# Kernel optimization log

Hardware: AMD Instinct MI355X
Metric: run time of the kernel (lower is better)

## Reference

```python
import jax, jax.numpy as jnp
import numpy as np
from jax import lax

# Quantization bit-widths per the module: QuantAct(16) on input,
# QuantConv2d(precision[0]=8), QuantAct(precision[0]+3=11) after relu1,
# QuantLinear(precision[1]=8).
INPUT_BIT = 16
CONV_W_BIT = 8
RELU_BIT = 11
DENSE_W_BIT = 8
EPS = 1e-8


def round_ste(x):
    # straight-through estimator rounding (HAWQ SymmetricQuantFunction)
    return x + lax.stop_gradient(jnp.round(x) - x)


def quant_act(x, bit):
    """Per-tensor symmetric dynamic activation quantization (HAWQ QuantAct).
    Returns fake-quantized x and its scaling factor."""
    n = 2 ** (bit - 1) - 1
    scale = lax.stop_gradient(jnp.maximum(jnp.max(jnp.abs(x)), EPS) / n)
    x_q = jnp.clip(round_ste(x / scale), -n, n) * scale
    return x_q, scale


def quant_weight(w, bit):
    """Per-output-channel symmetric weight quantization. w: [out, ...].
    Returns integer-valued weights and per-channel scale [out]."""
    n = 2 ** (bit - 1) - 1
    absmax = jnp.max(jnp.abs(w.reshape(w.shape[0], -1)), axis=1)
    sf = lax.stop_gradient(jnp.maximum(absmax, EPS) / n)
    bshape = (w.shape[0],) + (1,) * (w.ndim - 1)
    w_int = jnp.clip(round_ste(w / sf.reshape(bshape)), -n, n)
    return w_int, sf


def quant_conv2d(x, p_sf, w, b, bit, stride, pad):
    w_int, w_sf = quant_weight(w, bit)          # [O,I,kh,kw], [O]
    x_int = x / p_sf                            # integer-valued activations
    out_int = lax.conv_general_dilated(
        x_int, w_int, window_strides=(stride, stride),
        padding=((pad, pad), (pad, pad)),
        dimension_numbers=("NCHW", "OIHW", "NCHW"))
    bias_sf = p_sf * w_sf                       # [O]
    b_int = round_ste(b / bias_sf)
    out = (out_int + b_int[None, :, None, None]) * bias_sf[None, :, None, None]
    return out, w_sf


def quant_linear(x, p_sf, w, b, bit):
    w_int, w_sf = quant_weight(w, bit)          # [O,I], [O]
    x_int = x / p_sf
    bias_sf = p_sf * w_sf                       # [O]
    b_int = round_ste(b / bias_sf)
    out = (jnp.einsum("bi,oi->bo", x_int, w_int) + b_int[None, :]) * bias_sf[None, :]
    return out


def setup_inputs() -> dict:
    key = jax.random.key(0)
    k1, k2, k3, k4, k5 = jax.random.split(key, 5)
    B, Cin, H, W = 256, 3, 64, 64
    Cout, K = 64, 3
    Fin, Fout = Cout * 32 * 32, 256  # stride-2 conv -> 32x32 spatial
    x = jax.random.normal(k1, (B, Cin, H, W), dtype=jnp.float32)
    conv_w = jax.random.normal(k2, (Cout, Cin, K, K), dtype=jnp.float32) * 0.1
    conv_b = jax.random.normal(k3, (Cout,), dtype=jnp.float32) * 0.01
    dense_w = jax.random.normal(k4, (Fout, Fin), dtype=jnp.float32) * 0.02
    dense_b = jax.random.normal(k5, (Fout,), dtype=jnp.float32) * 0.01
    return {"x": x, "conv_w": conv_w, "conv_b": conv_b,
            "dense_w": dense_w, "dense_b": dense_b}


def reference(x, conv_w, conv_b, dense_w, dense_b):
    # x, p_sf = quant_input(x)
    xq, p_sf = quant_act(x, INPUT_BIT)
    # x, w_sf = conv(x, p_sf)
    h, w_sf = quant_conv2d(xq, p_sf, conv_w, conv_b, CONV_W_BIT, stride=2, pad=1)
    # relu1
    h = jax.nn.relu(h)
    # x, p_sf = quant_relu(x, p_sf, w_sf)  (requantize at relu_bit)
    h, p_sf = quant_act(h, RELU_BIT)
    # flatten
    h = h.reshape(h.shape[0], -1)
    # relu2(enc_dense(x, p_sf))
    out = jax.nn.relu(quant_linear(h, p_sf, dense_w, dense_b, DENSE_W_BIT))
    return out
```

## Files before the change

kernel.cpp:

```cpp
#include <hip/hip_runtime.h>
#include <hip/hip_fp16.h>
#include <cstdint>

#define B_   256
#define CIN  3
#define HW_  64
#define COUT 64
#define FIN  65536
#define FOUT 256

#define ACC_F    0
#define SC_F     65536
#define XPART_F  65552
#define WPART_F  66064
#define CSF_F    67088
#define CWINT_F  67152
#define H16_BYTE (512*1024)

typedef _Float16 half8  __attribute__((ext_vector_type(8)));
typedef _Float16 half4v __attribute__((ext_vector_type(4)));
typedef float    floatx4 __attribute__((ext_vector_type(4)));
typedef unsigned short u16;

__device__ inline float blockMax(float v) {
    #pragma unroll
    for (int off = 32; off; off >>= 1) v = fmaxf(v, __shfl_down(v, off));
    __shared__ float sm[8];
    const int lane = threadIdx.x & 63, w = threadIdx.x >> 6;
    if (lane == 0) sm[w] = v;
    __syncthreads();
    float m = sm[0];
    const int nw = blockDim.x >> 6;
    for (int i = 1; i < nw; i++) m = fmaxf(m, sm[i]);
    return m;
}

__global__ __launch_bounds__(256) void k_stats(const float* __restrict__ x,
                                               const float* __restrict__ dw,
                                               const float* __restrict__ cw,
                                               float* __restrict__ ws) {
    const int b = blockIdx.x;
    const int t = threadIdx.x;
    if (b < 512) {
        const float4* x4 = (const float4*)x;
        float m = 0.f;
        for (int i = b * 256 + t; i < (B_ * CIN * HW_ * HW_) / 4; i += 512 * 256) {
            float4 v = x4[i];
            m = fmaxf(m, fmaxf(fmaxf(fabsf(v.x), fabsf(v.y)), fmaxf(fabsf(v.z), fabsf(v.w))));
        }
        float bm = blockMax(m);
        if (t == 0) ws[XPART_F + b] = bm;
    } else if (b < 1536) {
        const int b2 = b - 512;
        const int row = b2 >> 2, q = b2 & 3;
        const float4* r = (const float4*)(dw + (size_t)row * FIN) + q * 4096;
        float m = 0.f;
        for (int i = t; i < 4096; i += 256) {
            float4 v = r[i];
            m = fmaxf(m, fmaxf(fmaxf(fabsf(v.x), fabsf(v.y)), fmaxf(fabsf(v.z), fabsf(v.w))));
        }
        float bm = blockMax(m);
        if (t == 0) ws[WPART_F + b2] = bm;
    } else if (b == 1536) {
        if (t == 64) ((unsigned*)ws)[SC_F + 1] = 0u;
        if (t < 64) {
            const int o = t;
            float wv[27];
            float m = 0.f;
            #pragma unroll
            for (int i = 0; i < 27; i++) { wv[i] = cw[o * 27 + i]; m = fmaxf(m, fabsf(wv[i])); }
            const float sf = fmaxf(m, 1e-8f) / 127.0f;
            #pragma unroll
            for (int i = 0; i < 27; i++)
                ws[CWINT_F + o * 27 + i] = fminf(127.f, fmaxf(-127.f, rintf(wv[i] / sf)));
            ws[CSF_F + o] = sf;
        }
    } else {
        ws[ACC_F + (b - 1537) * 256 + t] = 0.f;
    }
}

__global__ __launch_bounds__(256) void k_conv(const float* __restrict__ x,
                                              const float* __restrict__ cb,
                                              const float* __restrict__ ws,
                                              u16* __restrict__ h16,
                                              unsigned* __restrict__ maxh) {
    __shared__ float s_bsf[64], s_bint[64];
    __shared__ float xt[27 * 68];
    __shared__ float xp[256 * 28];
    const int t = threadIdx.x;

    float pm = fmaxf(ws[XPART_F + t], ws[XPART_F + 256 + t]);
    pm = blockMax(pm);
    const float p_sf = fmaxf(pm, 1e-8f) / 32767.0f;
    const float inv_p = 1.0f / p_sf;
    if (t < 64) {
        const float bsf = p_sf * ws[CSF_F + t];
        s_bsf[t]  = bsf;
        s_bint[t] = rintf(cb[t] / bsf);
    }

    const int b   = blockIdx.x >> 3;
    const int oyt = (blockIdx.x & 7) * 4;
    const float* xb = x + (size_t)b * (CIN * HW_ * HW_);

    for (int i = t; i < 432; i += 256) {
        const int lrow = i >> 4, c4 = i & 15;
        const int ci = lrow / 9, lr = lrow - ci * 9;
        const int iy = 2 * oyt - 1 + lr;
        float4 v = make_float4(0.f, 0.f, 0.f, 0.f);
        if ((unsigned)iy < 64u) v = *(const float4*)(xb + (ci * HW_ + iy) * HW_ + c4 * 4);
        float* d = &xt[lrow * 68 + 1 + c4 * 4];
        d[0] = fminf(32767.f, fmaxf(-32767.f, rintf(v.x * inv_p)));
        d[1] = fminf(32767.f, fmaxf(-32767.f, rintf(v.y * inv_p)));
        d[2] = fminf(32767.f, fmaxf(-32767.f, rintf(v.z * inv_p)));
        d[3] = fminf(32767.f, fmaxf(-32767.f, rintf(v.w * inv_p)));
    }
    if (t < 27) xt[t * 68] = 0.f;
    else if (t < 54) xt[(t - 27) * 68 + 65] = 0.f;
    __syncthreads();

    const int ox = t & 31;
    const int ch = __builtin_amdgcn_readfirstlane((t >> 6) & 1);
    const int dy = ((t >> 7) << 1) + ((t >> 5) & 1);
    const int oy = oyt + dy;

    float* myp = &xp[t * 28];
    #pragma unroll
    for (int ci = 0; ci < 3; ci++)
        #pragma unroll
        for (int ky = 0; ky < 3; ky++) {
            const float* rowp = &xt[(ci * 9 + 2 * dy + ky) * 68 + 2 * ox];
            #pragma unroll
            for (int kx = 0; kx < 3; kx++)
                myp[ci * 9 + ky * 3 + kx] = rowp[kx];
        }
    floatx4 xv0 = *(const floatx4*)(myp + 0);
    floatx4 xv1 = *(const floatx4*)(myp + 4);
    floatx4 xv2 = *(const floatx4*)(myp + 8);
    floatx4 xv3 = *(const floatx4*)(myp + 12);
    floatx4 xv4 = *(const floatx4*)(myp + 16);
    floatx4 xv5 = *(const floatx4*)(myp + 20);
    floatx4 xv6 = *(const floatx4*)(myp + 24);
    asm volatile("" : "+v"(xv0), "+v"(xv1), "+v"(xv2), "+v"(xv3),
                      "+v"(xv4), "+v"(xv5), "+v"(xv6));
    float xs[27];
    #pragma unroll
    for (int k = 0; k < 27; k++) {
        const int q = k >> 2, r = k & 3;
        xs[k] = (q == 0) ? xv0[r] : (q == 1) ? xv1[r] : (q == 2) ? xv2[r] :
                (q == 3) ? xv3[r] : (q == 4) ? xv4[r] : (q == 5) ? xv5[r] : xv6[r];
    }

    const float* wr = ws + CWINT_F + ch * (32 * 27);
    float mx = 0.f;
    u16* outp = h16 + (size_t)b * FIN + (size_t)ch * 32 * 1024 + oy * 32 + ox;

    float wbuf[27];
    #pragma unroll
    for (int k = 0; k < 27; k++) wbuf[k] = wr[k];
    #pragma unroll
    for (int c = 0; c < 32; c++) {
        float wcur[27];
        #pragma unroll
        for (int k = 0; k < 27; k++) wcur[k] = wbuf[k];
        if (c < 31) {
            const float* wn = wr + (c + 1) * 27;
            #pragma unroll
            for (int k = 0; k < 27; k++) wbuf[k] = wn[k];
        }
        float a = 0.f;
        #pragma unroll
        for (int k = 0; k < 27; k++) a = fmaf(xs[k], wcur[k], a);
        const int co = ch * 32 + c;
        float h = (a + s_bint[co]) * s_bsf[co];
        h = fmaxf(h, 0.f);
        mx = fmaxf(mx, h);
        outp[(size_t)c * 1024] = __half_as_ushort(__float2half(h));
    }
    float bm = blockMax(mx);
    if (t == 0) atomicMax(maxh, __float_as_uint(bm));
}

__global__ __launch_bounds__(256, 2) void k_gemm(const u16* __restrict__ h16,
                                                 const float* __restrict__ dw,
                                                 const float* __restrict__ ws,
                                                 float* __restrict__ accb) {
    __shared__ __align__(16) _Float16 As[128][72];
    __shared__ __align__(16) _Float16 Bs[128][72];
    __shared__ float invB[128];

    const int tid = threadIdx.x;
    const int tm  = (blockIdx.x >> 1) * 128;
    const int tn  = (blockIdx.x & 1) * 128;
    const int k0  = blockIdx.y * 512;

    const float max_h  = __uint_as_float(((const unsigned*)ws)[SC_F + 1]);
    const float p2     = fmaxf(max_h, 1e-8f) / 1023.0f;
    const float inv_p2 = 1.0f / p2;

    if (tid < 128) {
        const float* wp = ws + WPART_F + (size_t)(tn + tid) * 4;
        const float am = fmaxf(fmaxf(wp[0], wp[1]), fmaxf(wp[2], wp[3]));
        invB[tid] = 127.0f / fmaxf(am, 1e-8f);
    }

    floatx4 acc[4][4];
    const floatx4 zz = {0.f, 0.f, 0.f, 0.f};
    #pragma unroll
    for (int i = 0; i < 4; i++)
        #pragma unroll
        for (int j = 0; j < 4; j++) acc[i][j] = zz;

    const int wv = tid >> 6, lane = tid & 63;
    const int wm = (wv >> 1) * 64, wn = (wv & 1) * 64;
    const int lm = lane & 15, quad = lane >> 4;

    const int arow = tid >> 3, acol = tid & 7;
    const int brow = tid >> 4, bcol = tid & 15;

    half8  areg[4];
    float4 breg[8];

    #pragma unroll
    for (int r = 0; r < 4; r++)
        areg[r] = *(const half8*)(h16 + (size_t)(tm + arow + r * 32) * FIN + k0 + acol * 8);
    #pragma unroll
    for (int r = 0; r < 8; r++)
        breg[r] = *(const float4*)(dw + (size_t)(tn + brow + r * 16) * FIN + k0 + bcol * 4);

    __syncthreads();

    for (int kk = 0; kk < 8; kk++) {
        #pragma unroll
        for (int r = 0; r < 4; r++) {
            half8 qv;
            #pragma unroll
            for (int j = 0; j < 8; j++) {
                float f = (float)areg[r][j];
                qv[j] = (_Float16)fminf(1023.f, rintf(f * inv_p2));
            }
            *(half8*)&As[arow + r * 32][acol * 8] = qv;
        }
        #pragma unroll
        for (int r = 0; r < 8; r++) {
            const float is = invB[brow + r * 16];
            float4 v = breg[r];
            half4v qv;
            qv[0] = (_Float16)fminf(127.f, fmaxf(-127.f, rintf(v.x * is)));
            qv[1] = (_Float16)fminf(127.f, fmaxf(-127.f, rintf(v.y * is)));
            qv[2] = (_Float16)fminf(127.f, fmaxf(-127.f, rintf(v.z * is)));
            qv[3] = (_Float16)fminf(127.f, fmaxf(-127.f, rintf(v.w * is)));
            *(half4v*)&Bs[brow + r * 16][bcol * 4] = qv;
        }
        __syncthreads();

        if (kk < 7) {
            const int kn = k0 + (kk + 1) * 64;
            #pragma unroll
            for (int r = 0; r < 4; r++)
                areg[r] = *(const half8*)(h16 + (size_t)(tm + arow + r * 32) * FIN + kn + acol * 8);
            #pragma unroll
            for (int r = 0; r < 8; r++)
                breg[r] = *(const float4*)(dw + (size_t)(tn + brow + r * 16) * FIN + kn + bcol * 4);
        }

        #pragma unroll
        for (int ks = 0; ks < 2; ks++) {
            half8 af[4], bf[4];
            #pragma unroll
            for (int mi = 0; mi < 4; mi++)
                af[mi] = *(const half8*)&As[wm + mi * 16 + lm][ks * 32 + quad * 8];
            #pragma unroll
            for (int ni = 0; ni < 4; ni++)
                bf[ni] = *(const half8*)&Bs[wn + ni * 16 + lm][ks * 32 + quad * 8];
            #pragma unroll
            for (int mi = 0; mi < 4; mi++)
                #pragma unroll
                for (int ni = 0; ni < 4; ni++)
                    acc[mi][ni] = __builtin_amdgcn_mfma_f32_16x16x32_f16(af[mi], bf[ni], acc[mi][ni], 0, 0, 0);
        }
        __syncthreads();
    }

    #pragma unroll
    for (int mi = 0; mi < 4; mi++)
        #pragma unroll
        for (int ni = 0; ni < 4; ni++)
            #pragma unroll
            for (int r = 0; r < 4; r++) {
                const int row = tm + wm + mi * 16 + quad * 4 + r;
                const int col = tn + wn + ni * 16 + lm;
                atomicAdd(accb + row * FOUT + col, acc[mi][ni][r]);
            }
}

__global__ void k_epi(const float* __restrict__ accb, const float* __restrict__ db,
                      const float* __restrict__ ws, float* __restrict__ out) {
    const int idx = blockIdx.x * 256 + threadIdx.x;
    const int n = idx & 255;
    const float max_h = __uint_as_float(((const unsigned*)ws)[SC_F + 1]);
    const float p2 = fmaxf(max_h, 1e-8f) / 1023.0f;
    const float* wp = ws + WPART_F + (size_t)n * 4;
    const float am = fmaxf(fmaxf(fmaxf(wp[0], wp[1]), fmaxf(wp[2], wp[3])), 1e-8f);
    const float wsf = am / 127.0f;
    const float bsf = p2 * wsf;
    const float bint = rintf(db[n] / bsf);
    out[idx] = fmaxf(0.f, (accb[idx] + bint) * bsf);
}

extern "C" void kernel_launch(void* const* d_in, const int* in_sizes, int n_in,
                              void* d_out, int out_size, void* d_ws, size_t ws_size,
                              hipStream_t stream) {
    (void)in_sizes; (void)n_in; (void)out_size; (void)ws_size;
    const float* x  = (const float*)d_in[0];
    const float* cw = (const float*)d_in[1];
    const float* cb = (const float*)d_in[2];
    const float* dw = (const float*)d_in[3];
    const float* db = (const float*)d_in[4];
    float* out = (float*)d_out;
    float* ws  = (float*)d_ws;
    u16* h16   = (u16*)((char*)d_ws + H16_BYTE);
    float* accb = ws + ACC_F;
    unsigned* maxh = (unsigned*)ws + SC_F + 1;

    k_stats<<<1793, 256, 0, stream>>>(x, dw, cw, ws);
    k_conv<<<2048, 256, 0, stream>>>(x, cb, ws, h16, maxh);
    k_gemm<<<dim3(4, 128), 256, 0, stream>>>(h16, dw, ws, accb);
    k_epi<<<256, 256, 0, stream>>>(accb, db, ws, out);
}
```

Measured before the change: 198.0 us.

## Pre-quantize dense weights to int8 in stats kernel and double-buffer GEMM loads

```diff
diff --git a/kernel.cpp b/kernel.cpp
--- a/kernel.cpp
+++ b/kernel.cpp
@@ -16,11 +16,13 @@
 #define CSF_F    67088
 #define CWINT_F  67152
 #define H16_BYTE (512*1024)
+#define WQ_BYTE  (H16_BYTE + 256ll*FIN*2)
 
 typedef _Float16 half8  __attribute__((ext_vector_type(8)));
 typedef _Float16 half4v __attribute__((ext_vector_type(4)));
 typedef float    floatx4 __attribute__((ext_vector_type(4)));
 typedef unsigned short u16;
+typedef unsigned int uint_;
 
 __device__ inline float blockMax(float v) {
     #pragma unroll
@@ -38,7 +40,8 @@
 __global__ __launch_bounds__(256) void k_stats(const float* __restrict__ x,
                                                const float* __restrict__ dw,
                                                const float* __restrict__ cw,
-                                               float* __restrict__ ws) {
+                                               float* __restrict__ ws,
+                                               signed char* __restrict__ wq) {
     const int b = blockIdx.x;
     const int t = threadIdx.x;
     if (b < 512) {
@@ -50,18 +53,28 @@
         }
         float bm = blockMax(m);
         if (t == 0) ws[XPART_F + b] = bm;
-    } else if (b < 1536) {
-        const int b2 = b - 512;
-        const int row = b2 >> 2, q = b2 & 3;
-        const float4* r = (const float4*)(dw + (size_t)row * FIN) + q * 4096;
+    } else if (b < 768) {
+        const int row = b - 512;
+        const float4* r4 = (const float4*)(dw + (size_t)row * FIN);
         float m = 0.f;
-        for (int i = t; i < 4096; i += 256) {
-            float4 v = r[i];
+        for (int i = t; i < FIN / 4; i += 256) {
+            float4 v = r4[i];
             m = fmaxf(m, fmaxf(fmaxf(fabsf(v.x), fabsf(v.y)), fmaxf(fabsf(v.z), fabsf(v.w))));
         }
-        float bm = blockMax(m);
-        if (t == 0) ws[WPART_F + b2] = bm;
-    } else if (b == 1536) {
+        const float am = blockMax(m);
+        if (t == 0) ws[WPART_F + row] = am;
+        const float inv = 127.0f / fmaxf(am, 1e-8f);
+        uint_* wrow = (uint_*)(wq + (size_t)row * FIN);
+        for (int i = t; i < FIN / 4; i += 256) {
+            float4 v = r4[i];
+            int q0 = (int)fminf(127.f, fmaxf(-127.f, rintf(v.x * inv)));
+            int q1 = (int)fminf(127.f, fmaxf(-127.f, rintf(v.y * inv)));
+            int q2 = (int)fminf(127.f, fmaxf(-127.f, rintf(v.z * inv)));
+            int q3 = (int)fminf(127.f, fmaxf(-127.f, rintf(v.w * inv)));
+            wrow[i] = (uint_)(q0 & 255) | ((uint_)(q1 & 255) << 8) |
+                      ((uint_)(q2 & 255) << 16) | ((uint_)(q3 & 255) << 24);
+        }
+    } else if (b == 768) {
         if (t == 64) ((unsigned*)ws)[SC_F + 1] = 0u;
         if (t < 64) {
             const int o = t;
@@ -76,7 +89,7 @@
             ws[CSF_F + o] = sf;
         }
     } else {
-        ws[ACC_F + (b - 1537) * 256 + t] = 0.f;
+        ws[ACC_F + (b - 769) * 256 + t] = 0.f;
     }
 }
 
@@ -182,29 +195,35 @@
     if (t == 0) atomicMax(maxh, __float_as_uint(bm));
 }
 
-__global__ __launch_bounds__(256, 2) void k_gemm(const u16* __restrict__ h16,
-                                                 const float* __restrict__ dw,
-                                                 const float* __restrict__ ws,
-                                                 float* __restrict__ accb) {
+__device__ __forceinline__ half8 cvt_b8(uint_ lo, uint_ hi) {
+    half8 h;
+    h[0] = (_Float16)(float)(int)(signed char)(lo);
+    h[1] = (_Float16)(float)(int)(signed char)(lo >> 8);
+    h[2] = (_Float16)(float)(int)(signed char)(lo >> 16);
+    h[3] = (_Float16)(float)(int)(signed char)(lo >> 24);
+    h[4] = (_Float16)(float)(int)(signed char)(hi);
+    h[5] = (_Float16)(float)(int)(signed char)(hi >> 8);
+    h[6] = (_Float16)(float)(int)(signed char)(hi >> 16);
+    h[7] = (_Float16)(float)(int)(signed char)(hi >> 24);
+    return h;
+}
+
+__global__ __launch_bounds__(256) void k_gemm(const u16* __restrict__ h16,
+                                              const signed char* __restrict__ wq,
+                                              const float* __restrict__ ws,
+                                              float* __restrict__ accb) {
     __shared__ __align__(16) _Float16 As[128][72];
     __shared__ __align__(16) _Float16 Bs[128][72];
-    __shared__ float invB[128];
 
     const int tid = threadIdx.x;
     const int tm  = (blockIdx.x >> 1) * 128;
     const int tn  = (blockIdx.x & 1) * 128;
-    const int k0  = blockIdx.y * 512;
+    const int k0  = blockIdx.y * 1024;
 
     const float max_h  = __uint_as_float(((const unsigned*)ws)[SC_F + 1]);
     const float p2     = fmaxf(max_h, 1e-8f) / 1023.0f;
     const float inv_p2 = 1.0f / p2;
 
-    if (tid < 128) {
-        const float* wp = ws + WPART_F + (size_t)(tn + tid) * 4;
-        const float am = fmaxf(fmaxf(wp[0], wp[1]), fmaxf(wp[2], wp[3]));
-        invB[tid] = 127.0f / fmaxf(am, 1e-8f);
-    }
-
     floatx4 acc[4][4];
     const floatx4 zz = {0.f, 0.f, 0.f, 0.f};
     #pragma unroll
@@ -217,70 +236,55 @@
     const int lm = lane & 15, quad = lane >> 4;
 
     const int arow = tid >> 3, acol = tid & 7;
-    const int brow = tid >> 4, bcol = tid & 15;
-
-    half8  areg[4];
-    float4 breg[8];
-
-    #pragma unroll
-    for (int r = 0; r < 4; r++)
-        areg[r] = *(const half8*)(h16 + (size_t)(tm + arow + r * 32) * FIN + k0 + acol * 8);
-    #pragma unroll
-    for (int r = 0; r < 8; r++)
-        breg[r] = *(const float4*)(dw + (size_t)(tn + brow + r * 16) * FIN + k0 + bcol * 4);
-
-    __syncthreads();
-
-    for (int kk = 0; kk < 8; kk++) {
-        #pragma unroll
-        for (int r = 0; r < 4; r++) {
-            half8 qv;
-            #pragma unroll
-            for (int j = 0; j < 8; j++) {
-                float f = (float)areg[r][j];
-                qv[j] = (_Float16)fminf(1023.f, rintf(f * inv_p2));
-            }
-            *(half8*)&As[arow + r * 32][acol * 8] = qv;
-        }
-        #pragma unroll
-        for (int r = 0; r < 8; r++) {
-            const float is = invB[brow + r * 16];
-            float4 v = breg[r];
-            half4v qv;
-            qv[0] = (_Float16)fminf(127.f, fmaxf(-127.f, rintf(v.x * is)));
-            qv[1] = (_Float16)fminf(127.f, fmaxf(-127.f, rintf(v.y * is)));
-            qv[2] = (_Float16)fminf(127.f, fmaxf(-127.f, rintf(v.z * is)));
-            qv[3] = (_Float16)fminf(127.f, fmaxf(-127.f, rintf(v.w * is)));
-            *(half4v*)&Bs[brow + r * 16][bcol * 4] = qv;
-        }
-        __syncthreads();
-
-        if (kk < 7) {
-            const int kn = k0 + (kk + 1) * 64;
-            #pragma unroll
-            for (int r = 0; r < 4; r++)
-                areg[r] = *(const half8*)(h16 + (size_t)(tm + arow + r * 32) * FIN + kn + acol * 8);
-            #pragma unroll
-            for (int r = 0; r < 8; r++)
-                breg[r] = *(const float4*)(dw + (size_t)(tn + brow + r * 16) * FIN + kn + bcol * 4);
-        }
-
-        #pragma unroll
-        for (int ks = 0; ks < 2; ks++) {
-            half8 af[4], bf[4];
-            #pragma unroll
-            for (int mi = 0; mi < 4; mi++)
-                af[mi] = *(const half8*)&As[wm + mi * 16 + lm][ks * 32 + quad * 8];
-            #pragma unroll
-            for (int ni = 0; ni < 4; ni++)
-                bf[ni] = *(const half8*)&Bs[wn + ni * 16 + lm][ks * 32 + quad * 8];
-            #pragma unroll
-            for (int mi = 0; mi < 4; mi++)
-                #pragma unroll
-                for (int ni = 0; ni < 4; ni++)
-                    acc[mi][ni] = __builtin_amdgcn_mfma_f32_16x16x32_f16(af[mi], bf[ni], acc[mi][ni], 0, 0, 0);
-        }
-        __syncthreads();
+    const int brow = tid >> 1, bq   = (tid & 1) * 32;
+    const u16* abase = h16 + (size_t)(tm + arow) * FIN + k0 + acol * 8;
+    const signed char* bbase = wq + (size_t)(tn + brow) * FIN + k0 + bq;
+
+#define LOADA(dst, kk) { _Pragma("unroll") \
+    for (int r = 0; r < 4; r++) \
+        dst[r] = *(const half8*)(abase + (size_t)r * 32 * FIN + (kk) * 64); }
+#define LOADB(dst, kk) { const uint4* p_ = (const uint4*)(bbase + (kk) * 64); \
+    dst[0] = p_[0]; dst[1] = p_[1]; }
+#define STAGEA(src) { _Pragma("unroll") \
+    for (int r = 0; r < 4; r++) { half8 qv; _Pragma("unroll") \
+        for (int j = 0; j < 8; j++) { float f_ = (float)src[r][j]; \
+            qv[j] = (_Float16)fminf(1023.f, rintf(f_ * inv_p2)); } \
+        *(half8*)&As[arow + r * 32][acol * 8] = qv; } }
+#define STAGEB(src) { _Pragma("unroll") \
+    for (int u = 0; u < 2; u++) { uint4 wd_ = src[u]; \
+        *(half8*)&Bs[brow][bq + u * 16 + 0] = cvt_b8(wd_.x, wd_.y); \
+        *(half8*)&Bs[brow][bq + u * 16 + 8] = cvt_b8(wd_.z, wd_.w); } }
+#define BARRIER() do { asm volatile("s_waitcnt lgkmcnt(0)" ::: "memory"); \
+    __builtin_amdgcn_s_barrier(); } while (0)
+#define MFMA_PHASE() { _Pragma("unroll") \
+    for (int ks = 0; ks < 2; ks++) { half8 af[4], bf[4]; _Pragma("unroll") \
+        for (int mi = 0; mi < 4; mi++) \
+            af[mi] = *(const half8*)&As[wm + mi * 16 + lm][ks * 32 + quad * 8]; \
+        _Pragma("unroll") \
+        for (int ni = 0; ni < 4; ni++) \
+            bf[ni] = *(const half8*)&Bs[wn + ni * 16 + lm][ks * 32 + quad * 8]; \
+        _Pragma("unroll") \
+        for (int mi = 0; mi < 4; mi++) _Pragma("unroll") \
+            for (int ni = 0; ni < 4; ni++) \
+                acc[mi][ni] = __builtin_amdgcn_mfma_f32_16x16x32_f16(af[mi], bf[ni], acc[mi][ni], 0, 0, 0); } }
+
+    half8 a0[4], a1[4];
+    uint4 b0[2], b1[2];
+
+    LOADA(a0, 0); LOADB(b0, 0);
+    LOADA(a1, 1); LOADB(b1, 1);
+
+    for (int it = 0; it < 8; ++it) {
+        STAGEA(a0); STAGEB(b0);
+        if (it < 7) { LOADA(a0, 2 * it + 2); LOADB(b0, 2 * it + 2); }
+        BARRIER();
+        MFMA_PHASE();
+        BARRIER();
+        STAGEA(a1); STAGEB(b1);
+        if (it < 7) { LOADA(a1, 2 * it + 3); LOADB(b1, 2 * it + 3); }
+        BARRIER();
+        MFMA_PHASE();
+        BARRIER();
     }
 
     #pragma unroll
@@ -293,6 +297,12 @@
                 const int col = tn + wn + ni * 16 + lm;
                 atomicAdd(accb + row * FOUT + col, acc[mi][ni][r]);
             }
+#undef LOADA
+#undef LOADB
+#undef STAGEA
+#undef STAGEB
+#undef BARRIER
+#undef MFMA_PHASE
 }
 
 __global__ void k_epi(const float* __restrict__ accb, const float* __restrict__ db,
@@ -301,8 +311,7 @@
     const int n = idx & 255;
     const float max_h = __uint_as_float(((const unsigned*)ws)[SC_F + 1]);
     const float p2 = fmaxf(max_h, 1e-8f) / 1023.0f;
-    const float* wp = ws + WPART_F + (size_t)n * 4;
-    const float am = fmaxf(fmaxf(fmaxf(wp[0], wp[1]), fmaxf(wp[2], wp[3])), 1e-8f);
+    const float am = fmaxf(ws[WPART_F + n], 1e-8f);
     const float wsf = am / 127.0f;
     const float bsf = p2 * wsf;
     const float bint = rintf(db[n] / bsf);
@@ -321,11 +330,12 @@
     float* out = (float*)d_out;
     float* ws  = (float*)d_ws;
     u16* h16   = (u16*)((char*)d_ws + H16_BYTE);
+    signed char* wq = (signed char*)d_ws + WQ_BYTE;
     float* accb = ws + ACC_F;
     unsigned* maxh = (unsigned*)ws + SC_F + 1;
 
-    k_stats<<<1793, 256, 0, stream>>>(x, dw, cw, ws);
+    k_stats<<<1025, 256, 0, stream>>>(x, dw, cw, ws, wq);
     k_conv<<<2048, 256, 0, stream>>>(x, cb, ws, h16, maxh);
-    k_gemm<<<dim3(4, 128), 256, 0, stream>>>(h16, dw, ws, accb);
+    k_gemm<<<dim3(4, 64), 256, 0, stream>>>(h16, wq, ws, accb);
     k_epi<<<256, 256, 0, stream>>>(accb, db, ws, out);
 }
```

After: 209.2 us. +5.7%, slower.
